# Performance work log

Hardware: AMD Instinct MI355X
Metric: run time of the kernel (lower is better)

Reference implementation:

```python
import jax, jax.numpy as jnp
import numpy as np

EMBED = 1024
HEADS = 16
HEAD_DIM = EMBED // HEADS


def setup_inputs() -> dict:
    key = jax.random.key(0)
    ks = jax.random.split(key, 8)
    N, S = 4, 2048
    values = jax.random.normal(ks[0], (N, S, EMBED), dtype=jnp.float32)
    queries = jax.random.normal(ks[1], (N, S, EMBED), dtype=jnp.float32)
    keys = jax.random.normal(ks[2], (N, S, EMBED), dtype=jnp.float32)
    mask = jax.random.randint(ks[3], (N, 1, S, S), 0, 2, dtype=jnp.int32)
    sc = 1.0 / np.sqrt(HEAD_DIM)
    Wv = jax.random.normal(ks[4], (HEAD_DIM, HEAD_DIM), dtype=jnp.float32) * sc
    Wk = jax.random.normal(ks[5], (HEAD_DIM, HEAD_DIM), dtype=jnp.float32) * sc
    Wq = jax.random.normal(ks[6], (HEAD_DIM, HEAD_DIM), dtype=jnp.float32) * sc
    Wo = jax.random.normal(ks[7], (EMBED, EMBED), dtype=jnp.float32) * (1.0 / np.sqrt(EMBED))
    bo = jnp.zeros((EMBED,), dtype=jnp.float32)
    return {"values": values, "queries": queries, "keys": keys, "mask": mask,
            "Wv": Wv, "Wk": Wk, "Wq": Wq, "Wo": Wo, "bo": bo}


def reference(values, queries, keys, mask, Wv, Wk, Wq, Wo, bo):
    N, S, _ = queries.shape
    # split heads: (N, len, H, D)
    v = values.reshape(N, -1, HEADS, HEAD_DIM)
    k = keys.reshape(N, -1, HEADS, HEAD_DIM)
    q = queries.reshape(N, -1, HEADS, HEAD_DIM)
    # per-head linear projections (nn.Linear: y = x @ W.T, no bias)
    v = jnp.einsum('nlhd,ed->nlhe', v, Wv)
    k = jnp.einsum('nlhd,ed->nlhe', k, Wk)
    q = jnp.einsum('nlhd,ed->nlhe', q, Wq)
    # energy: (N, H, q_len, k_len)
    energy = jnp.einsum('nqhd,nkhd->nhqk', q, k)
    energy = jnp.where(mask == 0, jnp.float32(-1e20), energy)
    # non-standard scale: sqrt(embed_size), applied after masking
    attn = jax.nn.softmax(energy / jnp.sqrt(jnp.float32(EMBED)), axis=3)
    out = jnp.einsum('nhql,nlhd->nqhd', attn, v).reshape(N, S, EMBED)
    return out @ Wo.T + bo
```

## Files before the change

### kernel.cpp

```cpp
#include <hip/hip_runtime.h>
#include <hip/hip_bf16.h>

#define NBATCH 4
#define SEQ    2048
#define EMBED  1024
#define HEADS  16
#define HD     64

typedef __attribute__((ext_vector_type(8))) short bf16x8;
typedef __attribute__((ext_vector_type(4))) float f32x4;
typedef __attribute__((ext_vector_type(16))) float f32x16;

__device__ __forceinline__ short f2bf(float f) {
  union { float f; unsigned u; } v; v.f = f;
  unsigned r = v.u + 0x7fffu + ((v.u >> 16) & 1u);
  return (short)(r >> 16);
}

__device__ __forceinline__ unsigned pkbf(float a, float b) {
#if __has_builtin(__builtin_amdgcn_cvt_pk_bf16_f32)
  typedef __attribute__((ext_vector_type(2))) __bf16 bf16x2_t;
  bf16x2_t r = __builtin_amdgcn_cvt_pk_bf16_f32(a, b);
  union { bf16x2_t v; unsigned u; } cv; cv.v = r; return cv.u;
#else
  return (unsigned)(unsigned short)f2bf(a) | ((unsigned)(unsigned short)f2bf(b) << 16);
#endif
}

typedef __attribute__((address_space(1))) const void gas_void;
typedef __attribute__((address_space(3))) void las_void;
__device__ __forceinline__ void glds16(const void* g, void* l) {
  __builtin_amdgcn_global_load_lds((gas_void*)g, (las_void*)l, 16, 0, 0);
}

__device__ __forceinline__ bf16x8 mk8(unsigned a, unsigned b, unsigned c, unsigned d) {
  union { unsigned u[4]; bf16x8 v; } t;
  t.u[0] = a; t.u[1] = b; t.u[2] = c; t.u[3] = d; return t.v;
}

__device__ __forceinline__ void pl32swap(unsigned &a, unsigned &b) {
  asm volatile("v_permlane32_swap_b32 %0, %1" : "+v"(a), "+v"(b));
}

#define MFMA32(A, B, C) __builtin_amdgcn_mfma_f32_32x32x16_bf16((A), (B), (C), 0, 0, 0)

#define C2 0.04508422f

__global__ __launch_bounds__(256) void cvt_all(
    const float* __restrict__ Wo, const float* __restrict__ Wq,
    const float* __restrict__ Wk, const float* __restrict__ Wv,
    short* __restrict__ dWo, short* __restrict__ dWq,
    short* __restrict__ dWk, short* __restrict__ dWv)
{
  int e = (blockIdx.x * 256 + threadIdx.x) * 4;
  const float* src; short* dst; int off; float sc = 1.0f;
  if (e < EMBED * EMBED) { src = Wo; dst = dWo; off = e; }
  else {
    int j = e - EMBED * EMBED;
    if      (j < 4096)  { src = Wq; dst = dWq; off = j; sc = C2; }
    else if (j < 8192)  { src = Wk; dst = dWk; off = j - 4096; }
    else if (j < 12288) { src = Wv; dst = dWv; off = j - 8192; }
    else return;
  }
  float4 v = *(const float4*)(src + off);
  ushort4 p;
  p.x = (unsigned short)f2bf(v.x * sc);
  p.y = (unsigned short)f2bf(v.y * sc);
  p.z = (unsigned short)f2bf(v.z * sc);
  p.w = (unsigned short)f2bf(v.w * sc);
  *(ushort4*)(dst + off) = p;
}

__global__ __launch_bounds__(256) void mask_pack(const int* __restrict__ mask,
                                                 unsigned long long* __restrict__ bits) {
  long long t = (long long)blockIdx.x * 256 + threadIdx.x;
  int lane = threadIdx.x & 63;
  int m = mask[t];
  unsigned long long b = __ballot(m != 0);
  if (lane == 0) bits[t >> 6] = b;
}

__global__ __launch_bounds__(256) void proj_kernel(
    const float* __restrict__ srcQ, const float* __restrict__ srcK, const float* __restrict__ srcV,
    const short* __restrict__ WbQ, const short* __restrict__ WbK, const short* __restrict__ WbV,
    short* __restrict__ Qp, short* __restrict__ Kp, short* __restrict__ Vt)
{
  int rt = blockIdx.x;
  int h  = blockIdx.y;
  int mz = blockIdx.z;
  const float* src = (mz == 0) ? srcQ : ((mz == 1) ? srcK : srcV);
  const short* Wb  = (mz == 0) ? WbQ : ((mz == 1) ? WbK : WbV);

  __shared__ __align__(16) short At[64][72];

  int tid = threadIdx.x;
  int r0 = rt * 64;
  for (int idx = tid; idx < 64 * 16; idx += 256) {
    int row = idx >> 4;
    int c4  = idx & 15;
    float4 v = *(const float4*)(src + (long long)(r0 + row) * EMBED + h * HD + c4 * 4);
    uint2 pk2;
    pk2.x = pkbf(v.x, v.y);
    pk2.y = pkbf(v.z, v.w);
    *(uint2*)&At[row][c4 * 4] = pk2;
  }
  __syncthreads();

  int lane = tid & 63, w = tid >> 6, quad = lane >> 4, l15 = lane & 15;

  bf16x8 af0 = *(const bf16x8*)&At[w * 16 + l15][quad * 8];
  bf16x8 af1 = *(const bf16x8*)&At[w * 16 + l15][32 + quad * 8];

  f32x4 acc[4];
  for (int cg = 0; cg < 4; cg++) {
    acc[cg] = (f32x4){0.f, 0.f, 0.f, 0.f};
    bf16x8 b0 = *(const bf16x8*)(Wb + (cg * 16 + l15) * 64 + quad * 8);
    bf16x8 b1 = *(const bf16x8*)(Wb + (cg * 16 + l15) * 64 + 32 + quad * 8);
    acc[cg] = __builtin_amdgcn_mfma_f32_16x16x32_bf16(af0, b0, acc[cg], 0, 0, 0);
    acc[cg] = __builtin_amdgcn_mfma_f32_16x16x32_bf16(af1, b1, acc[cg], 0, 0, 0);
  }

  int rloc = w * 16 + quad * 4;
  __syncthreads();
  if (mz < 2) {
#pragma unroll
    for (int cg = 0; cg < 4; cg++)
#pragma unroll
      for (int reg = 0; reg < 4; reg++)
        At[rloc + reg][cg * 16 + l15] = f2bf(acc[cg][reg]);
  } else {
#pragma unroll
    for (int cg = 0; cg < 4; cg++)
#pragma unroll
      for (int reg = 0; reg < 4; reg++)
        At[cg * 16 + l15][rloc + reg] = f2bf(acc[cg][reg]);
  }
  __syncthreads();

  short* dst = (mz == 0) ? Qp : ((mz == 1) ? Kp : Vt);
  int row2 = tid >> 2, ch = tid & 3;
  const uint4* lp = (const uint4*)&At[row2][ch * 16];
  uint4 v0 = lp[0], v1 = lp[1];
  char* g;
  if (mz < 2) {
    int r = r0 + row2; int n = r >> 11, s = r & 2047;
    g = (char*)(dst + ((long long)(n * HEADS + h) * SEQ + s) * HD) + ch * 32;
  } else {
    int n = r0 >> 11, s0 = r0 & 2047;
    g = (char*)(dst + ((long long)(n * HEADS + h) * HD + row2) * SEQ + s0) + ch * 32;
  }
  *(uint4*)g = v0;
  *(uint4*)(g + 16) = v1;
}

#define SOFTMAX_KK(SV, MW, PAV0, PAV1) do {                                       \
    unsigned n0 = ((MW) >> sh4) & 0xFu;                                           \
    unsigned n1 = ((MW) >> (sh4 + 8)) & 0xFu;                                     \
    unsigned n2 = ((MW) >> (sh4 + 16)) & 0xFu;                                    \
    unsigned n3 = ((MW) >> (sh4 + 24)) & 0xFu;                                    \
    float p0  = __builtin_amdgcn_exp2f(SV[0]);   p0  = (n0 & 1u) ? p0  : 0.f;     \
    float p1  = __builtin_amdgcn_exp2f(SV[1]);   p1  = (n0 & 2u) ? p1  : 0.f;     \
    float p2  = __builtin_amdgcn_exp2f(SV[2]);   p2  = (n0 & 4u) ? p2  : 0.f;     \
    float p3  = __builtin_amdgcn_exp2f(SV[3]);   p3  = (n0 & 8u) ? p3  : 0.f;     \
    float p4  = __builtin_amdgcn_exp2f(SV[4]);   p4  = (n1 & 1u) ? p4  : 0.f;     \
    float p5  = __builtin_amdgcn_exp2f(SV[5]);   p5  = (n1 & 2u) ? p5  : 0.f;     \
    float p6  = __builtin_amdgcn_exp2f(SV[6]);   p6  = (n1 & 4u) ? p6  : 0.f;     \
    float p7  = __builtin_amdgcn_exp2f(SV[7]);   p7  = (n1 & 8u) ? p7  : 0.f;     \
    float p8  = __builtin_amdgcn_exp2f(SV[8]);   p8  = (n2 & 1u) ? p8  : 0.f;     \
    float p9  = __builtin_amdgcn_exp2f(SV[9]);   p9  = (n2 & 2u) ? p9  : 0.f;     \
    float p10 = __builtin_amdgcn_exp2f(SV[10]);  p10 = (n2 & 4u) ? p10 : 0.f;     \
    float p11 = __builtin_amdgcn_exp2f(SV[11]);  p11 = (n2 & 8u) ? p11 : 0.f;     \
    float p12 = __builtin_amdgcn_exp2f(SV[12]);  p12 = (n3 & 1u) ? p12 : 0.f;     \
    float p13 = __builtin_amdgcn_exp2f(SV[13]);  p13 = (n3 & 2u) ? p13 : 0.f;     \
    float p14 = __builtin_amdgcn_exp2f(SV[14]);  p14 = (n3 & 4u) ? p14 : 0.f;     \
    float p15 = __builtin_amdgcn_exp2f(SV[15]);  p15 = (n3 & 8u) ? p15 : 0.f;     \
    lsum += (((p0 + p1) + (p2 + p3)) + ((p4 + p5) + (p6 + p7)))                   \
          + (((p8 + p9) + (p10 + p11)) + ((p12 + p13) + (p14 + p15)));            \
    unsigned u0 = pkbf(p0, p1),   u1 = pkbf(p2, p3);                              \
    unsigned u2 = pkbf(p4, p5),   u3 = pkbf(p6, p7);                              \
    unsigned u4 = pkbf(p8, p9),   u5 = pkbf(p10, p11);                            \
    unsigned u6 = pkbf(p12, p13), u7 = pkbf(p14, p15);                            \
    pl32swap(u0, u2); pl32swap(u1, u3);                                           \
    pl32swap(u4, u6); pl32swap(u5, u7);                                           \
    PAV0 = mk8(u0, u1, u2, u3);                                                   \
    PAV1 = mk8(u4, u5, u6, u7);                                                   \
  } while (0)

#define ATTN_ITER(BUF, KT) do {                                                   \
    __syncthreads();                                                              \
    if ((KT) < 31) {                                                              \
      const char* ks_ = Kb + ((KT) + 1) * 8192 + kgo;                             \
      const char* vs_ = Vb + ((KT) + 1) * 128 + vgo;                              \
      char* kd_ = ldsK + (((BUF) ^ 1) * 8192) + klo;                              \
      char* vd_ = ldsV + (((BUF) ^ 1) * 8192) + klo;                              \
      glds16(ks_,          kd_);                                                  \
      glds16(ks_ + 4096,   kd_ + 4096);                                           \
      glds16(vs_,          vd_);                                                  \
      glds16(vs_ + 131072, vd_ + 4096);                                           \
      mnxt = mptr[(KT) + 1];                                                      \
    }                                                                             \
    unsigned mlo = (unsigned)mcur, mhiw = (unsigned)(mcur >> 32);                 \
    const char* KB_ = ldsK + (BUF) * 8192;                                        \
    const char* VB_ = ldsV + (BUF) * 8192;                                        \
    bf16x8 pa0, pa1, pa2, pa3;                                                    \
    {                                                                             \
      f32x16 s = {};                                                              \
      __builtin_amdgcn_s_setprio(1);                                              \
      s = MFMA32(*(const bf16x8*)(KB_ + a4_0), qf0, s);                           \
      s = MFMA32(*(const bf16x8*)(KB_ + a4_1), qf1, s);                           \
      s = MFMA32(*(const bf16x8*)(KB_ + a4_2), qf2, s);                           \
      s = MFMA32(*(const bf16x8*)(KB_ + a4_3), qf3, s);                           \
      __builtin_amdgcn_s_setprio(0);                                              \
      SOFTMAX_KK(s, mlo, pa0, pa1);                                               \
    }                                                                             \
    {                                                                             \
      f32x16 s = {};                                                              \
      __builtin_amdgcn_s_setprio(1);                                              \
      s = MFMA32(*(const bf16x8*)(KB_ + 4096 + a4_0), qf0, s);                    \
      s = MFMA32(*(const bf16x8*)(KB_ + 4096 + a4_1), qf1, s);                    \
      s = MFMA32(*(const bf16x8*)(KB_ + 4096 + a4_2), qf2, s);                    \
      s = MFMA32(*(const bf16x8*)(KB_ + 4096 + a4_3), qf3, s);                    \
      __builtin_amdgcn_s_setprio(0);                                              \
      SOFTMAX_KK(s, mhiw, pa2, pa3);                                              \
    }                                                                             \
    __builtin_amdgcn_s_setprio(1);                                                \
    O0 = MFMA32(*(const bf16x8*)(VB_ + a4_0),        pa0, O0);                    \
    O1 = MFMA32(*(const bf16x8*)(VB_ + 4096 + a4_0), pa0, O1);                    \
    O0 = MFMA32(*(const bf16x8*)(VB_ + a4_1),        pa1, O0);                    \
    O1 = MFMA32(*(const bf16x8*)(VB_ + 4096 + a4_1), pa1, O1);                    \
    O0 = MFMA32(*(const bf16x8*)(VB_ + a4_2),        pa2, O0);                    \
    O1 = MFMA32(*(const bf16x8*)(VB_ + 4096 + a4_2), pa2, O1);                    \
    O0 = MFMA32(*(const bf16x8*)(VB_ + a4_3),        pa3, O0);                    \
    O1 = MFMA32(*(const bf16x8*)(VB_ + 4096 + a4_3), pa3, O1);                    \
    __builtin_amdgcn_s_setprio(0);                                                \
    mcur = mnxt;                                                                  \
  } while (0)

__global__ __launch_bounds__(256, 3) void attn_kernel(
    const short* __restrict__ Qp, const short* __restrict__ Kp, const short* __restrict__ Vt,
    const unsigned long long* __restrict__ mbits, short* __restrict__ AO)
{
  int L  = blockIdx.x;
  int qt = (L >> 3) & 15;
  int p_ = ((L >> 7) << 3) | (L & 7);
  int h  = p_ & 15;
  int nb = p_ >> 4;
  int q0 = qt * 128;

  __shared__ __align__(16) char ldsK[2 * 8192];
  __shared__ __align__(16) char ldsV[2 * 8192];

  int tid = threadIdx.x, lane = tid & 63, w = tid >> 6;
  int l31 = lane & 31, hi5 = lane >> 5;
  int g8 = lane & 7, r8 = lane >> 3;
  int pp = lane & 7;
  unsigned sh4 = (unsigned)(hi5 * 4);

  long long nh = (long long)(nb * HEADS + h);
  const char* Kb = (const char*)(Kp + nh * SEQ * HD);
  const char* Vb = (const char*)(Vt + nh * HD * SEQ);

  int kgo = (w * 8 + r8) * 128 + ((g8 ^ r8) << 4);
  int vgo = (w * 8 + r8) * 4096 + ((g8 ^ r8) << 4);
  int klo = w * 1024;

  int a4_0 = l31 * 128 + ((((0 | hi5) ^ pp)) << 4);
  int a4_1 = l31 * 128 + ((((2 | hi5) ^ pp)) << 4);
  int a4_2 = l31 * 128 + ((((4 | hi5) ^ pp)) << 4);
  int a4_3 = l31 * 128 + ((((6 | hi5) ^ pp)) << 4);

  int qrow = q0 + w * 32 + l31;
  const short* Qb = Qp + (nh * SEQ + qrow) * HD + hi5 * 8;
  bf16x8 qf0 = *(const bf16x8*)(Qb);
  bf16x8 qf1 = *(const bf16x8*)(Qb + 16);
  bf16x8 qf2 = *(const bf16x8*)(Qb + 32);
  bf16x8 qf3 = *(const bf16x8*)(Qb + 48);

  const unsigned long long* mptr = mbits + ((long long)nb * SEQ + qrow) * 32;

  f32x16 O0 = {}, O1 = {};
  float lsum = 0.f;

  glds16(Kb + kgo,          ldsK + klo);
  glds16(Kb + 4096 + kgo,   ldsK + 4096 + klo);
  glds16(Vb + vgo,          ldsV + klo);
  glds16(Vb + vgo + 131072, ldsV + 4096 + klo);
  unsigned long long mcur = mptr[0], mnxt = 0;

  for (int it = 0; it < 16; it++) {
    ATTN_ITER(0, it * 2);
    ATTN_ITER(1, it * 2 + 1);
  }

  lsum += __shfl_xor(lsum, 32);
  float inv = 1.f / lsum;

  short* aoRow = AO + ((long long)nb * SEQ + qrow) * EMBED + h * HD + hi5 * 4;
#pragma unroll
  for (int j = 0; j < 4; j++) {
    uint2 pk;
    pk.x = pkbf(O0[4 * j] * inv, O0[4 * j + 1] * inv);
    pk.y = pkbf(O0[4 * j + 2] * inv, O0[4 * j + 3] * inv);
    *(uint2*)(aoRow + j * 8) = pk;
    pk.x = pkbf(O1[4 * j] * inv, O1[4 * j + 1] * inv);
    pk.y = pkbf(O1[4 * j + 2] * inv, O1[4 * j + 3] * inv);
    *(uint2*)(aoRow + 32 + j * 8) = pk;
  }
}

__global__ __launch_bounds__(512) void outproj_kernel(
    const short* __restrict__ AO, const short* __restrict__ Wob,
    const float* __restrict__ bo, float* __restrict__ out)
{
  int rt = blockIdx.x, ct = blockIdx.y;
  __shared__ __align__(16) short AtL[128 * 64];
  __shared__ __align__(16) short BtL[128 * 64];

  int tid = threadIdx.x, lane = tid & 63, w = tid >> 6, quad = lane >> 4, l15 = lane & 15;
  int r8b = tid >> 3, g8 = tid & 7;
  int swz = g8 ^ (r8b & 7);
  int s3 = l15 & 7;
  int o0 = (quad ^ s3) * 16;
  int o1 = ((quad + 4) ^ s3) * 16;

  int r0 = rt * 128, c0 = ct * 128;
  int wr = (w >> 1) * 32, wc = (w & 1) * 64;

  const char* Abase = (const char*)AO  + (long long)(r0 + r8b) * 2048 + swz * 16;
  const char* Bbase = (const char*)Wob + (long long)(c0 + r8b) * 2048 + swz * 16;
  unsigned lbase = (unsigned)tid * 16;

  f32x4 acc[2][4];
#pragma unroll
  for (int mi = 0; mi < 2; mi++)
#pragma unroll
    for (int ni = 0; ni < 4; ni++) acc[mi][ni] = (f32x4){0.f, 0.f, 0.f, 0.f};

  for (int kc = 0; kc < 16; kc++) {
    __syncthreads();
    glds16(Abase + kc * 128,                 (char*)AtL + lbase);
    glds16(Abase + 64LL * 2048 + kc * 128,   (char*)AtL + lbase + 8192);
    glds16(Bbase + kc * 128,                 (char*)BtL + lbase);
    glds16(Bbase + 64LL * 2048 + kc * 128,   (char*)BtL + lbase + 8192);
    __syncthreads();

    const char* AB = (const char*)AtL;
    const char* BB = (const char*)BtL;
    bf16x8 af[2][2];
#pragma unroll
    for (int mi = 0; mi < 2; mi++) {
      int r = wr + mi * 16 + l15;
      af[mi][0] = *(const bf16x8*)(AB + r * 128 + o0);
      af[mi][1] = *(const bf16x8*)(AB + r * 128 + o1);
    }
#pragma unroll
    for (int ni = 0; ni < 4; ni++) {
      int r = wc + ni * 16 + l15;
      bf16x8 b0 = *(const bf16x8*)(BB + r * 128 + o0);
      bf16x8 b1 = *(const bf16x8*)(BB + r * 128 + o1);
#pragma unroll
      for (int mi = 0; mi < 2; mi++) {
        acc[mi][ni] = __builtin_amdgcn_mfma_f32_16x16x32_bf16(af[mi][0], b0, acc[mi][ni], 0, 0, 0);
        acc[mi][ni] = __builtin_amdgcn_mfma_f32_16x16x32_bf16(af[mi][1], b1, acc[mi][ni], 0, 0, 0);
      }
    }
  }

#pragma unroll
  for (int ni = 0; ni < 4; ni++) {
    float b = bo[c0 + wc + ni * 16 + l15];
#pragma unroll
    for (int mi = 0; mi < 2; mi++)
#pragma unroll
      for (int reg = 0; reg < 4; reg++) {
        int r = r0 + wr + mi * 16 + quad * 4 + reg;
        out[(long long)r * EMBED + c0 + wc + ni * 16 + l15] = acc[mi][ni][reg] + b;
      }
  }
}

extern "C" void kernel_launch(void* const* d_in, const int* in_sizes, int n_in,
                              void* d_out, int out_size, void* d_ws, size_t ws_size,
                              hipStream_t stream) {
  const float* values  = (const float*)d_in[0];
  const float* queries = (const float*)d_in[1];
  const float* keys    = (const float*)d_in[2];
  const int*   mask    = (const int*)d_in[3];
  const float* Wv = (const float*)d_in[4];
  const float* Wk = (const float*)d_in[5];
  const float* Wq = (const float*)d_in[6];
  const float* Wo = (const float*)d_in[7];
  const float* bo = (const float*)d_in[8];
  float* out = (float*)d_out;

  char* ws = (char*)d_ws;
  size_t off = 0;
  const size_t PROJ_BYTES = (size_t)NBATCH * HEADS * SEQ * HD * 2;
  short* Qp = (short*)(ws + off); off += PROJ_BYTES;
  short* Kp = (short*)(ws + off); off += PROJ_BYTES;
  short* Vt = (short*)(ws + off); off += PROJ_BYTES;
  short* AO = (short*)(ws + off); off += PROJ_BYTES;
  unsigned long long* mbits = (unsigned long long*)(ws + off);
  off += (size_t)NBATCH * SEQ * (SEQ / 64) * 8;
  short* Wob = (short*)(ws + off); off += (size_t)EMBED * EMBED * 2;
  short* WbQ = (short*)(ws + off); off += HD * HD * 2;
  short* WbK = (short*)(ws + off); off += HD * HD * 2;
  short* WbV = (short*)(ws + off); off += HD * HD * 2;

  cvt_all<<<dim3((EMBED * EMBED + 3 * HD * HD) / 4 / 256), dim3(256), 0, stream>>>(
      Wo, Wq, Wk, Wv, Wob, WbQ, WbK, WbV);

  mask_pack<<<dim3((NBATCH * SEQ * SEQ) / 256), dim3(256), 0, stream>>>(mask, mbits);

  proj_kernel<<<dim3((NBATCH * SEQ) / 64, HEADS, 3), dim3(256), 0, stream>>>(
      queries, keys, values, WbQ, WbK, WbV, Qp, Kp, Vt);

  attn_kernel<<<dim3(SEQ / 128 * HEADS * NBATCH), dim3(256), 0, stream>>>(Qp, Kp, Vt, mbits, AO);

  outproj_kernel<<<dim3((NBATCH * SEQ) / 128, EMBED / 128), dim3(512), 0, stream>>>(AO, Wob, bo, out);
}
```

Baseline: 367.7 us.

## Batch mask packing, double-buffer outproj loads, split attention launch, reuse zero accumulator

The mask packing kernel now has each thread handle four elements and write the ballot words as 16-byte stores, cutting the block count and store traffic. The output projection double-buffers its LDS tiles, prefetching the next K chunk during the current MFMAs, and raises wave priority around the matrix ops. The attention kernel starts each score accumulation from a zero vector held in registers instead of rematerialising zeros. Attention is also split into two launches over batch halves, which adds launch overhead and gives each launch fewer blocks.

```diff
diff --git a/kernel.cpp b/kernel.cpp
--- a/kernel.cpp
+++ b/kernel.cpp
@@ -73,11 +73,21 @@
 
 __global__ __launch_bounds__(256) void mask_pack(const int* __restrict__ mask,
                                                  unsigned long long* __restrict__ bits) {
-  long long t = (long long)blockIdx.x * 256 + threadIdx.x;
-  int lane = threadIdx.x & 63;
-  int m = mask[t];
-  unsigned long long b = __ballot(m != 0);
-  if (lane == 0) bits[t >> 6] = b;
+  long long base = (long long)blockIdx.x * 1024;
+  int tid = threadIdx.x, lane = tid & 63, wv = tid >> 6;
+  const int* p = mask + base + wv * 256 + lane;
+  int m0 = p[0], m1 = p[64], m2 = p[128], m3 = p[192];
+  unsigned long long b0 = __ballot(m0 != 0);
+  unsigned long long b1 = __ballot(m1 != 0);
+  unsigned long long b2 = __ballot(m2 != 0);
+  unsigned long long b3 = __ballot(m3 != 0);
+  if (lane == 0) {
+    unsigned long long* d = bits + (base >> 6) + wv * 4;
+    ulonglong2 w0; w0.x = b0; w0.y = b1;
+    ulonglong2 w1; w1.x = b2; w1.y = b3;
+    *(ulonglong2*)(d)     = w0;
+    *(ulonglong2*)(d + 2) = w1;
+  }
 }
 
 __global__ __launch_bounds__(256) void proj_kernel(
@@ -204,9 +214,8 @@
     const char* VB_ = ldsV + (BUF) * 8192;                                        \
     bf16x8 pa0, pa1, pa2, pa3;                                                    \
     {                                                                             \
-      f32x16 s = {};                                                              \
       __builtin_amdgcn_s_setprio(1);                                              \
-      s = MFMA32(*(const bf16x8*)(KB_ + a4_0), qf0, s);                           \
+      f32x16 s = MFMA32(*(const bf16x8*)(KB_ + a4_0), qf0, zc);                   \
       s = MFMA32(*(const bf16x8*)(KB_ + a4_1), qf1, s);                           \
       s = MFMA32(*(const bf16x8*)(KB_ + a4_2), qf2, s);                           \
       s = MFMA32(*(const bf16x8*)(KB_ + a4_3), qf3, s);                           \
@@ -214,9 +223,8 @@
       SOFTMAX_KK(s, mlo, pa0, pa1);                                               \
     }                                                                             \
     {                                                                             \
-      f32x16 s = {};                                                              \
       __builtin_amdgcn_s_setprio(1);                                              \
-      s = MFMA32(*(const bf16x8*)(KB_ + 4096 + a4_0), qf0, s);                    \
+      f32x16 s = MFMA32(*(const bf16x8*)(KB_ + 4096 + a4_0), qf0, zc);            \
       s = MFMA32(*(const bf16x8*)(KB_ + 4096 + a4_1), qf1, s);                    \
       s = MFMA32(*(const bf16x8*)(KB_ + 4096 + a4_2), qf2, s);                    \
       s = MFMA32(*(const bf16x8*)(KB_ + 4096 + a4_3), qf3, s);                    \
@@ -238,13 +246,13 @@
 
 __global__ __launch_bounds__(256, 3) void attn_kernel(
     const short* __restrict__ Qp, const short* __restrict__ Kp, const short* __restrict__ Vt,
-    const unsigned long long* __restrict__ mbits, short* __restrict__ AO)
+    const unsigned long long* __restrict__ mbits, short* __restrict__ AO, int nbase)
 {
   int L  = blockIdx.x;
   int qt = (L >> 3) & 15;
   int p_ = ((L >> 7) << 3) | (L & 7);
   int h  = p_ & 15;
-  int nb = p_ >> 4;
+  int nb = nbase + (p_ >> 4);
   int q0 = qt * 128;
 
   __shared__ __align__(16) char ldsK[2 * 8192];
@@ -277,6 +285,9 @@
   bf16x8 qf3 = *(const bf16x8*)(Qb + 48);
 
   const unsigned long long* mptr = mbits + ((long long)nb * SEQ + qrow) * 32;
+
+  f32x16 zc = {};
+  asm volatile("" : "+v"(zc));
 
   f32x16 O0 = {}, O1 = {};
   float lsum = 0.f;
@@ -313,8 +324,8 @@
     const float* __restrict__ bo, float* __restrict__ out)
 {
   int rt = blockIdx.x, ct = blockIdx.y;
-  __shared__ __align__(16) short AtL[128 * 64];
-  __shared__ __align__(16) short BtL[128 * 64];
+  __shared__ __align__(16) short AtL[2][128 * 64];
+  __shared__ __align__(16) short BtL[2][128 * 64];
 
   int tid = threadIdx.x, lane = tid & 63, w = tid >> 6, quad = lane >> 4, l15 = lane & 15;
   int r8b = tid >> 3, g8 = tid & 7;
@@ -336,16 +347,24 @@
 #pragma unroll
     for (int ni = 0; ni < 4; ni++) acc[mi][ni] = (f32x4){0.f, 0.f, 0.f, 0.f};
 
+  glds16(Abase,               (char*)AtL[0] + lbase);
+  glds16(Abase + 64LL * 2048, (char*)AtL[0] + lbase + 8192);
+  glds16(Bbase,               (char*)BtL[0] + lbase);
+  glds16(Bbase + 64LL * 2048, (char*)BtL[0] + lbase + 8192);
+
   for (int kc = 0; kc < 16; kc++) {
     __syncthreads();
-    glds16(Abase + kc * 128,                 (char*)AtL + lbase);
-    glds16(Abase + 64LL * 2048 + kc * 128,   (char*)AtL + lbase + 8192);
-    glds16(Bbase + kc * 128,                 (char*)BtL + lbase);
-    glds16(Bbase + 64LL * 2048 + kc * 128,   (char*)BtL + lbase + 8192);
-    __syncthreads();
-
-    const char* AB = (const char*)AtL;
-    const char* BB = (const char*)BtL;
+    const char* AB = (const char*)AtL[kc & 1];
+    const char* BB = (const char*)BtL[kc & 1];
+    if (kc < 15) {
+      char* dA = (char*)AtL[(kc & 1) ^ 1] + lbase;
+      char* dB = (char*)BtL[(kc & 1) ^ 1] + lbase;
+      glds16(Abase + (kc + 1) * 128,               dA);
+      glds16(Abase + 64LL * 2048 + (kc + 1) * 128, dA + 8192);
+      glds16(Bbase + (kc + 1) * 128,               dB);
+      glds16(Bbase + 64LL * 2048 + (kc + 1) * 128, dB + 8192);
+    }
+
     bf16x8 af[2][2];
 #pragma unroll
     for (int mi = 0; mi < 2; mi++) {
@@ -353,6 +372,7 @@
       af[mi][0] = *(const bf16x8*)(AB + r * 128 + o0);
       af[mi][1] = *(const bf16x8*)(AB + r * 128 + o1);
     }
+    __builtin_amdgcn_s_setprio(1);
 #pragma unroll
     for (int ni = 0; ni < 4; ni++) {
       int r = wc + ni * 16 + l15;
@@ -364,6 +384,7 @@
         acc[mi][ni] = __builtin_amdgcn_mfma_f32_16x16x32_bf16(af[mi][1], b1, acc[mi][ni], 0, 0, 0);
       }
     }
+    __builtin_amdgcn_s_setprio(0);
   }
 
 #pragma unroll
@@ -410,12 +431,13 @@
   cvt_all<<<dim3((EMBED * EMBED + 3 * HD * HD) / 4 / 256), dim3(256), 0, stream>>>(
       Wo, Wq, Wk, Wv, Wob, WbQ, WbK, WbV);
 
-  mask_pack<<<dim3((NBATCH * SEQ * SEQ) / 256), dim3(256), 0, stream>>>(mask, mbits);
+  mask_pack<<<dim3((NBATCH * SEQ * SEQ) / 1024), dim3(256), 0, stream>>>(mask, mbits);
 
   proj_kernel<<<dim3((NBATCH * SEQ) / 64, HEADS, 3), dim3(256), 0, stream>>>(
       queries, keys, values, WbQ, WbK, WbV, Qp, Kp, Vt);
 
-  attn_kernel<<<dim3(SEQ / 128 * HEADS * NBATCH), dim3(256), 0, stream>>>(Qp, Kp, Vt, mbits, AO);
+  attn_kernel<<<dim3(512), dim3(256), 0, stream>>>(Qp, Kp, Vt, mbits, AO, 0);
+  attn_kernel<<<dim3(512), dim3(256), 0, stream>>>(Qp, Kp, Vt, mbits, AO, 2);
 
   outproj_kernel<<<dim3((NBATCH * SEQ) / 128, EMBED / 128), dim3(512), 0, stream>>>(AO, Wob, bo, out);
 }
```

Result: no change. 369.2 us (+0.4%).
